# Performance work log

Hardware: AMD Instinct MI355X
Metric: run time of the kernel (lower is better)

## Reference

```python
import jax, jax.numpy as jnp
import numpy as np

VALID_THRESH = 0.001


def setup_inputs() -> dict:
    key = jax.random.key(0)
    k1, k2 = jax.random.split(key)
    B, H, W = 2, 64, 192
    vals = jax.random.uniform(k1, (B, 1, H, W), dtype=jnp.float32)
    mask = (jax.random.uniform(k2, (B, 1, H, W)) < 0.05).astype(jnp.float32)
    S = vals * mask
    yy, xx = jnp.meshgrid(jnp.arange(H, dtype=jnp.float32),
                          jnp.arange(W, dtype=jnp.float32), indexing='ij')
    return {"S": S, "xx": xx, "yy": yy, "num": 4}


def _dist_forward(S, xx, yy, num):
    B, _, H, W = S.shape
    N = H * W
    Sf = S.reshape(B, N)
    valid = Sf > VALID_THRESH                      # [B, N]
    xy = jnp.stack([xx.reshape(-1), yy.reshape(-1)], axis=0).astype(jnp.float32)  # [2, N]

    def per_batch(v):
        # squared distance from each query pixel n to each candidate pixel m
        dx = xy[0][:, None] - xy[0][None, :]       # [N, N]
        dy = xy[1][:, None] - xy[1][None, :]
        d = dx * dx + dy * dy
        d = jnp.where(v[None, :], d, jnp.inf)      # mask out invalid candidates
        _, args = jax.lax.top_k(-d, num)           # [N, num] global pixel indices of k nearest valid pts
        # offsets of the k nearest valid points relative to each query pixel
        ipc = (xy[:, args] - xy[:, :, None])       # [2, N, num]
        return ipc.transpose(0, 2, 1), args.T      # [2, num, N], [num, N]

    IPCnum, args = jax.lax.map(per_batch, valid)   # [B,2,num,N], [B,num,N]
    return IPCnum, args


def reference(S, xx, yy, num):
    return _dist_forward(S, xx, yy, num)
```

## Files before the change

### kernel.cpp

```cpp
#include <hip/hip_runtime.h>
#include <hip/hip_bf16.h>
#include <limits.h>

constexpr int W = 192;
constexpr int H = 64;
constexpr int N = H * W;
constexpr int B = 2;
constexpr int NUM = 4;
constexpr float THRESH = 0.001f;
constexpr int SLICES = 8;
constexpr int QPB = 64;
constexpr int THREADS = SLICES * QPB;
constexpr int CH = 1024;
constexpr int PAD = 0x3FFFFFFF;

__global__ void compact_kernel(const float* __restrict__ S, int* __restrict__ ws) {
    const int b = blockIdx.y;
    const int i0 = (blockIdx.x * 256 + threadIdx.x) * 4;
    const float4 v = *(const float4*)(S + b * N + i0);
    int* lb = ws + 16 + b * N;
    const int lane = threadIdx.x & 63;
#pragma unroll
    for (int j = 0; j < 4; ++j) {
        const int i = i0 + j;
        const float val = (j == 0) ? v.x : (j == 1) ? v.y : (j == 2) ? v.z : v.w;
        const bool valid = val > THRESH;
        const unsigned long long mask = __ballot(valid);
        const int cnt = __popcll(mask);
        int base = 0;
        if (lane == 0 && cnt) base = atomicAdd(&ws[b], cnt);
        base = __shfl(base, 0);
        if (valid) {
            const int pos = base + __popcll(mask & ((1ull << lane) - 1ull));
            const int ym = i / W;
            const int xm = i - ym * W;
            lb[pos] = xm | (ym << 8) | (i << 16);
        }
    }
}

#define INSERT(key, K0, K1, K2, K3) do {            \
    int _t = max((key), K0); K0 = min((key), K0);   \
    int _u = max(_t, K1);    K1 = min(_t, K1);      \
    int _v = max(_u, K2);    K2 = min(_u, K2);      \
    K3 = min(_v, K3);                               \
} while (0)

#define PROC(p, K0, K1, K2, K3) do {                \
    const int _xm = (p) & 255;                      \
    const int _ym = ((p) >> 8) & 255;               \
    const int _dx = _xm - xn;                       \
    const int _dy = _ym - yn;                       \
    const int _d = __mul24(_dx, _dx) + __mul24(_dy, _dy); \
    const int _key = (_d << 14) | ((p) >> 16);      \
    INSERT(_key, K0, K1, K2, K3);                   \
} while (0)

__global__ __launch_bounds__(THREADS) void knn_kernel(const int* __restrict__ ws,
                                                      float* __restrict__ out) {
    const int b = blockIdx.y;
    const int q = threadIdx.x & (QPB - 1);
    const int s = threadIdx.x >> 6;
    const int n = blockIdx.x * QPB + q;
    const int yn = n / W;
    const int xn = n - yn * W;
    const int V = ws[b];
    const int* lb = ws + 16 + b * N;

    __shared__ int cand[CH];
    __shared__ int keym[NUM][THREADS];

    int k0 = INT_MAX, k1 = INT_MAX, k2 = INT_MAX, k3 = INT_MAX;
    int a0 = INT_MAX, a1 = INT_MAX, a2 = INT_MAX, a3 = INT_MAX;

    for (int base = 0; base < V; base += CH) {
        const int c = min(CH, V - base);
        const int cpad = (c + 2 * SLICES - 1) & ~(2 * SLICES - 1);
        __syncthreads();
        for (int i = threadIdx.x; i < c; i += THREADS) cand[i] = lb[base + i];
        for (int i = c + threadIdx.x; i < cpad; i += THREADS) cand[i] = PAD;
        __syncthreads();
        for (int i = s * 2; i < cpad; i += SLICES * 2) {
            const int pA = cand[i];
            const int pB = cand[i + 1];
            PROC(pA, k0, k1, k2, k3);
            PROC(pB, a0, a1, a2, a3);
        }
    }
    INSERT(a0, k0, k1, k2, k3);
    INSERT(a1, k0, k1, k2, k3);
    INSERT(a2, k0, k1, k2, k3);
    INSERT(a3, k0, k1, k2, k3);

    keym[0][threadIdx.x] = k0;
    keym[1][threadIdx.x] = k1;
    keym[2][threadIdx.x] = k2;
    keym[3][threadIdx.x] = k3;
    __syncthreads();

    if (s == 0) {
#pragma unroll
        for (int sl = 1; sl < SLICES; ++sl) {
#pragma unroll
            for (int k = 0; k < NUM; ++k) {
                const int key = keym[k][sl * QPB + q];
                INSERT(key, k0, k1, k2, k3);
            }
        }
        const int keys[NUM] = {k0, k1, k2, k3};
        float* argout = out + (size_t)B * 2 * NUM * N;
#pragma unroll
        for (int k = 0; k < NUM; ++k) {
            const int m = keys[k] & 16383;
            const int ym = m / W;
            const int xm = m - ym * W;
            out[(((b * 2 + 0) * NUM + k) * N) + n] = (float)(xm - xn);
            out[(((b * 2 + 1) * NUM + k) * N) + n] = (float)(ym - yn);
            argout[(b * NUM + k) * N + n] = (float)m;
        }
    }
}

extern "C" void kernel_launch(void* const* d_in, const int* in_sizes, int n_in,
                              void* d_out, int out_size, void* d_ws, size_t ws_size,
                              hipStream_t stream) {
    const float* S = (const float*)d_in[0];
    float* out = (float*)d_out;
    int* ws = (int*)d_ws;

    hipMemsetAsync(ws, 0, 64, stream);
    compact_kernel<<<dim3(N / 1024, B), dim3(256), 0, stream>>>(S, ws);
    knn_kernel<<<dim3(N / QPB, B), dim3(THREADS), 0, stream>>>(ws, out);
}
```

Measured before the change: 78.14 us.

## Fuse compaction into kNN kernel, each block compacting valid points into LDS

```diff
diff --git a/kernel.cpp b/kernel.cpp
--- a/kernel.cpp
+++ b/kernel.cpp
@@ -11,33 +11,7 @@
 constexpr int SLICES = 8;
 constexpr int QPB = 64;
 constexpr int THREADS = SLICES * QPB;
-constexpr int CH = 1024;
 constexpr int PAD = 0x3FFFFFFF;
-
-__global__ void compact_kernel(const float* __restrict__ S, int* __restrict__ ws) {
-    const int b = blockIdx.y;
-    const int i0 = (blockIdx.x * 256 + threadIdx.x) * 4;
-    const float4 v = *(const float4*)(S + b * N + i0);
-    int* lb = ws + 16 + b * N;
-    const int lane = threadIdx.x & 63;
-#pragma unroll
-    for (int j = 0; j < 4; ++j) {
-        const int i = i0 + j;
-        const float val = (j == 0) ? v.x : (j == 1) ? v.y : (j == 2) ? v.z : v.w;
-        const bool valid = val > THRESH;
-        const unsigned long long mask = __ballot(valid);
-        const int cnt = __popcll(mask);
-        int base = 0;
-        if (lane == 0 && cnt) base = atomicAdd(&ws[b], cnt);
-        base = __shfl(base, 0);
-        if (valid) {
-            const int pos = base + __popcll(mask & ((1ull << lane) - 1ull));
-            const int ym = i / W;
-            const int xm = i - ym * W;
-            lb[pos] = xm | (ym << 8) | (i << 16);
-        }
-    }
-}
 
 #define INSERT(key, K0, K1, K2, K3) do {            \
     int _t = max((key), K0); K0 = min((key), K0);   \
@@ -56,36 +30,59 @@
     INSERT(_key, K0, K1, K2, K3);                   \
 } while (0)
 
-__global__ __launch_bounds__(THREADS) void knn_kernel(const int* __restrict__ ws,
-                                                      float* __restrict__ out) {
+__global__ __launch_bounds__(THREADS) void dist_kernel(const float* __restrict__ S,
+                                                       float* __restrict__ out) {
     const int b = blockIdx.y;
     const int q = threadIdx.x & (QPB - 1);
     const int s = threadIdx.x >> 6;
     const int n = blockIdx.x * QPB + q;
     const int yn = n / W;
     const int xn = n - yn * W;
-    const int V = ws[b];
-    const int* lb = ws + 16 + b * N;
+    const int lane = threadIdx.x & 63;
 
-    __shared__ int cand[CH];
+    __shared__ int cand[N];
     __shared__ int keym[NUM][THREADS];
+    __shared__ int sh_cnt;
+
+    if (threadIdx.x == 0) sh_cnt = 0;
+    __syncthreads();
+
+    const float* Sb = S + b * N;
+#pragma unroll
+    for (int k = 0; k < N / (THREADS * 4); ++k) {
+        const int i0 = (k * THREADS + threadIdx.x) * 4;
+        const float4 v = *(const float4*)(Sb + i0);
+#pragma unroll
+        for (int j = 0; j < 4; ++j) {
+            const int i = i0 + j;
+            const float val = (j == 0) ? v.x : (j == 1) ? v.y : (j == 2) ? v.z : v.w;
+            const bool valid = val > THRESH;
+            const unsigned long long mask = __ballot(valid);
+            const int cnt = __popcll(mask);
+            int base = 0;
+            if (lane == 0 && cnt) base = atomicAdd(&sh_cnt, cnt);
+            base = __shfl(base, 0);
+            if (valid) {
+                const int pos = base + __popcll(mask & ((1ull << lane) - 1ull));
+                const int ym = i / W;
+                const int xm = i - ym * W;
+                cand[pos] = xm | (ym << 8) | (i << 16);
+            }
+        }
+    }
+    __syncthreads();
+    const int V = sh_cnt;
+    const int Vpad = (V + 2 * SLICES - 1) & ~(2 * SLICES - 1);
+    for (int i = V + threadIdx.x; i < Vpad; i += THREADS) cand[i] = PAD;
+    __syncthreads();
 
     int k0 = INT_MAX, k1 = INT_MAX, k2 = INT_MAX, k3 = INT_MAX;
     int a0 = INT_MAX, a1 = INT_MAX, a2 = INT_MAX, a3 = INT_MAX;
-
-    for (int base = 0; base < V; base += CH) {
-        const int c = min(CH, V - base);
-        const int cpad = (c + 2 * SLICES - 1) & ~(2 * SLICES - 1);
-        __syncthreads();
-        for (int i = threadIdx.x; i < c; i += THREADS) cand[i] = lb[base + i];
-        for (int i = c + threadIdx.x; i < cpad; i += THREADS) cand[i] = PAD;
-        __syncthreads();
-        for (int i = s * 2; i < cpad; i += SLICES * 2) {
-            const int pA = cand[i];
-            const int pB = cand[i + 1];
-            PROC(pA, k0, k1, k2, k3);
-            PROC(pB, a0, a1, a2, a3);
-        }
+    for (int i = s * 2; i < Vpad; i += SLICES * 2) {
+        const int pA = cand[i];
+        const int pB = cand[i + 1];
+        PROC(pA, k0, k1, k2, k3);
+        PROC(pB, a0, a1, a2, a3);
     }
     INSERT(a0, k0, k1, k2, k3);
     INSERT(a1, k0, k1, k2, k3);
@@ -126,9 +123,5 @@
                               hipStream_t stream) {
     const float* S = (const float*)d_in[0];
     float* out = (float*)d_out;
-    int* ws = (int*)d_ws;
-
-    hipMemsetAsync(ws, 0, 64, stream);
-    compact_kernel<<<dim3(N / 1024, B), dim3(256), 0, stream>>>(S, ws);
-    knn_kernel<<<dim3(N / QPB, B), dim3(THREADS), 0, stream>>>(ws, out);
+    dist_kernel<<<dim3(N / QPB, B), dim3(THREADS), 0, stream>>>(S, out);
 }
```

Measured after the change: 73.88 us. -5.4%, faster.
